# Performance work log

Hardware: AMD Instinct MI355X
Metric: run time of the kernel (lower is better)

The kernel has to match this reference:

```python
import jax, jax.numpy as jnp
import numpy as np

K = 30          # hard-coded in Hypergraph.from_feature_kNN(ft, k=30)
BN_EPS = 1e-5   # BatchNorm1d eval mode, running_mean=0, running_var=1


def setup_inputs() -> dict:
    key = jax.random.key(0)
    ks = jax.random.split(key, 3)
    B, C, H, W = 8, 64, 56, 56
    hid = 32
    return {
        "x": jax.random.normal(ks[0], (B, C, H, W), jnp.float32),
        "w1": jax.random.normal(ks[1], (C, hid), jnp.float32) / np.sqrt(C).astype(np.float32),
        "b1": jnp.zeros((hid,), jnp.float32),
        "g1": jnp.ones((hid,), jnp.float32),
        "be1": jnp.zeros((hid,), jnp.float32),
        "w2": jax.random.normal(ks[2], (hid, C), jnp.float32) / np.sqrt(hid).astype(np.float32),
        "b2": jnp.zeros((C,), jnp.float32),
        "g2": jnp.ones((C,), jnp.float32),
        "be2": jnp.zeros((C,), jnp.float32),
    }


def _knn_idx(ft, k):
    # squared euclidean distances via gram trick; same ordering as torch.cdist
    sq = jnp.sum(ft * ft, axis=1)
    d2 = sq[:, None] + sq[None, :] - 2.0 * (ft @ ft.T)   # [L, L]
    _, idx = jax.lax.top_k(-d2, k)                        # k smallest distances (incl. self)
    return idx                                            # [L, k] -> hyperedge e = kNN of vertex e


def _v2v_mean(X, nbr):
    # hg.v2v(X, aggr="mean"): v2e mean then e2v mean over the kNN incidence structure
    L, k = nbr.shape
    F = X.shape[1]
    Y = jnp.mean(X[nbr], axis=1)                                        # v2e: [L_edges, F]
    seg = nbr.reshape(-1)                                               # vertex nbr[e,j] belongs to edge e
    vals = jnp.broadcast_to(Y[:, None, :], (L, k, F)).reshape(L * k, F)
    s = jax.ops.segment_sum(vals, seg, num_segments=L)                  # e2v sum
    dv = jax.ops.segment_sum(jnp.ones((L * k,), X.dtype), seg, num_segments=L)
    return s / jnp.maximum(dv, 1.0)[:, None]                            # e2v mean


def _bn_eval(x, g, b):
    # BatchNorm1d in eval: running_mean=0, running_var=1
    return x * (g * np.float32(1.0 / np.sqrt(1.0 + BN_EPS))) + b


def reference(x, w1, b1, g1, be1, w2, b2, g2, be2):
    B, C, H, W = x.shape
    L = H * W
    xf = x.reshape(B, L, C)  # faithful raw x.view(B, L, C) (no transpose in source)

    def per_sample(ft):
        nbr = _knn_idx(ft, K)
        # HGNNPConv 1: theta -> bn -> v2v(mean) -> relu (dropout off in eval)
        h = _bn_eval(ft @ w1 + b1, g1, be1)
        h = jax.nn.relu(_v2v_mean(h, nbr))
        # HGNNPConv 2 (is_last): theta -> bn -> v2v(mean), no act/drop
        h = _bn_eval(h @ w2 + b2, g2, be2)
        return _v2v_mean(h, nbr)  # [L, C]

    outs = jax.vmap(per_sample)(xf)      # [B, L, C]
    return outs.reshape(B, -1, H, W)     # faithful raw outs.view(B, -1, H, W)
```

## Files before the change

kernel.cpp:

```cpp
#include <hip/hip_runtime.h>
#include <math.h>


namespace {

constexpr int cB = 8;
constexpr int cL = 3136;
constexpr int cC = 64;
constexpr int cH = 32;
constexpr int cK = 30;
constexpr int NV = cB * cL;
constexpr int QD = 10;
constexpr float BN_SC = 0.99999500003749964f;

typedef __bf16 bf16x8 __attribute__((ext_vector_type(8)));
typedef float floatx4 __attribute__((ext_vector_type(4)));

union BU {
  __bf16 b[2];
  unsigned u;
};

__device__ inline unsigned umin2(unsigned a, unsigned b) { return a < b ? a : b; }
__device__ inline unsigned umax2(unsigned a, unsigned b) { return a > b ? a : b; }
__device__ inline unsigned umin3(unsigned a, unsigned b, unsigned c) {
  return umin2(umin2(a, b), c);
}
__device__ inline float bf16lo(unsigned u) { return __uint_as_float(u << 16); }
__device__ inline float bf16hi(unsigned u) {
  return __uint_as_float(u & 0xFFFF0000u);
}

__device__ inline unsigned bclean64(unsigned v, int ln) {
#pragma unroll
  for (int off = 32; off; off >>= 1) {
    unsigned p = (unsigned)__shfl_xor((int)v, off);
    v = (ln & off) ? umax2(v, p) : umin2(v, p);
  }
  return v;
}

__global__ __launch_bounds__(256) void k_splitth(
    const float* __restrict__ x, const float* __restrict__ w1,
    const float* __restrict__ b1, const float* __restrict__ g1,
    const float* __restrict__ be1, ushort* __restrict__ xhi,
    ushort* __restrict__ xlo, float* __restrict__ sqf,
    int* __restrict__ cnt, int* __restrict__ cur, __bf16* __restrict__ h1) {
  __shared__ float w1s[cC * cH];
  __shared__ float xs[8 * 64];
  const int t = threadIdx.x;
  const int v0 = blockIdx.x * 8;
  for (int n = t; n < cC * cH; n += 256) w1s[n] = w1[n];
  {
    float2 xv = reinterpret_cast<const float2*>(x + (size_t)v0 * 64)[t];
    xs[2 * t] = xv.x;
    xs[2 * t + 1] = xv.y;
    BU hh, ll;
    hh.b[0] = (__bf16)xv.x;
    hh.b[1] = (__bf16)xv.y;
    ll.b[0] = (__bf16)(xv.x - (float)hh.b[0]);
    ll.b[1] = (__bf16)(xv.y - (float)hh.b[1]);
    reinterpret_cast<unsigned*>(xhi)[(size_t)v0 * 32 + t] = hh.u;
    reinterpret_cast<unsigned*>(xlo)[(size_t)v0 * 32 + t] = ll.u;
    float ss = xv.x * xv.x + xv.y * xv.y;
#pragma unroll
    for (int off = 1; off < 32; off <<= 1) ss += __shfl_xor(ss, off);
    if ((t & 31) == 0) sqf[v0 + (t >> 5)] = ss * 1024.f + 262144.f;
  }
  if (t < 8) {
    cnt[v0 + t] = 0;
    cur[v0 + t] = 0;
  }
  __syncthreads();
  const int r = t >> 5, f = t & 31;
  float s = 0.f;
#pragma unroll
  for (int k = 0; k < cC; ++k) s = fmaf(xs[r * 64 + k], w1s[k * cH + f], s);
  h1[(size_t)(v0 + r) * cH + f] =
      (__bf16)((s + b1[f]) * (g1[f] * BN_SC) + be1[f]);
}

__global__ __launch_bounds__(128, 4) void k_sweep(
    const ushort* __restrict__ xhi, const ushort* __restrict__ xlo,
    const float* __restrict__ sqf, unsigned* __restrict__ candq) {
  const int ib = blockIdx.x, qt = blockIdx.y, b = blockIdx.z;
  const int r0 = ib * 32;
  const int jb0 = qt * 1568;
  const int ntile = 49;
  const size_t bbase = (size_t)b * cL;

  __shared__ ushort aHi[32 * 72], aLo[32 * 72];
  __shared__ ushort bHi[32 * 72], bLo[32 * 72];
  __shared__ float sqJs[32];

  const int t  = threadIdx.x;
  const int ln = t & 63;
  const int w  = t >> 6;
  const int tx = ln & 15;
  const int qd = ln >> 4;

#pragma unroll
  for (int it = 0; it < 2; ++it) {
    int idx = t + 128 * it;
    int r = idx >> 3, blk = idx & 7;
    *reinterpret_cast<uint4*>(&aHi[r * 72 + blk * 8]) =
        *reinterpret_cast<const uint4*>(&xhi[(bbase + r0 + r) * 64 + blk * 8]);
    *reinterpret_cast<uint4*>(&aLo[r * 72 + blk * 8]) =
        *reinterpret_cast<const uint4*>(&xlo[(bbase + r0 + r) * 64 + blk * 8]);
  }
  __syncthreads();

  bf16x8 aH[2], aL[2];
#pragma unroll
  for (int kk = 0; kk < 2; ++kk) {
    aH[kk] = *reinterpret_cast<const bf16x8*>(
        &aHi[(w * 16 + tx) * 72 + kk * 32 + qd * 8]);
    aL[kk] = *reinterpret_cast<const bf16x8*>(
        &aLo[(w * 16 + tx) * 72 + kk * 32 + qd * 8]);
  }

  unsigned q[4][QD];
#pragma unroll
  for (int e = 0; e < 4; ++e)
#pragma unroll
    for (int k = 0; k < QD; ++k) q[e][k] = 0xFFFFFFFFu;

  const int pr  = (t + 0)   >> 3, pblk  = (t + 0)   & 7;
  const int pr1 = (t + 128) >> 3, pblk1 = (t + 128) & 7;
  uint4 pH0, pH1, pL0, pL1;
  float pS = 0.f;
  {
    const int jb = jb0;
    pH0 = *reinterpret_cast<const uint4*>(&xhi[(bbase + jb + pr) * 64 + pblk * 8]);
    pL0 = *reinterpret_cast<const uint4*>(&xlo[(bbase + jb + pr) * 64 + pblk * 8]);
    pH1 = *reinterpret_cast<const uint4*>(&xhi[(bbase + jb + pr1) * 64 + pblk1 * 8]);
    pL1 = *reinterpret_cast<const uint4*>(&xlo[(bbase + jb + pr1) * 64 + pblk1 * 8]);
    if (t < 32) pS = sqf[bbase + jb + t];
  }

  for (int st = 0; st < ntile; ++st) {
    __syncthreads();
    *reinterpret_cast<uint4*>(&bHi[pr * 72 + pblk * 8])   = pH0;
    *reinterpret_cast<uint4*>(&bLo[pr * 72 + pblk * 8])   = pL0;
    *reinterpret_cast<uint4*>(&bHi[pr1 * 72 + pblk1 * 8]) = pH1;
    *reinterpret_cast<uint4*>(&bLo[pr1 * 72 + pblk1 * 8]) = pL1;
    if (t < 32) sqJs[t] = pS;
    __syncthreads();

    if (st + 1 < ntile) {
      const int jb = jb0 + (st + 1) * 32;
      pH0 = *reinterpret_cast<const uint4*>(&xhi[(bbase + jb + pr) * 64 + pblk * 8]);
      pL0 = *reinterpret_cast<const uint4*>(&xlo[(bbase + jb + pr) * 64 + pblk * 8]);
      pH1 = *reinterpret_cast<const uint4*>(&xhi[(bbase + jb + pr1) * 64 + pblk1 * 8]);
      pL1 = *reinterpret_cast<const uint4*>(&xlo[(bbase + jb + pr1) * 64 + pblk1 * 8]);
      if (t < 32) pS = sqf[bbase + jb + t];
    }
    __builtin_amdgcn_sched_barrier(0);

    unsigned pk[2][4];
#pragma unroll
    for (int f = 0; f < 2; ++f) {
      const int bro = (f * 16 + tx) * 72 + qd * 8;
      bf16x8 bh0 = *reinterpret_cast<const bf16x8*>(&bHi[bro]);
      bf16x8 bh1 = *reinterpret_cast<const bf16x8*>(&bHi[bro + 32]);
      bf16x8 bl0 = *reinterpret_cast<const bf16x8*>(&bLo[bro]);
      bf16x8 bl1 = *reinterpret_cast<const bf16x8*>(&bLo[bro + 32]);
      floatx4 acc = {0.f, 0.f, 0.f, 0.f};
      acc = __builtin_amdgcn_mfma_f32_16x16x32_bf16(aH[0], bh0, acc, 0, 0, 0);
      acc = __builtin_amdgcn_mfma_f32_16x16x32_bf16(aH[1], bh1, acc, 0, 0, 0);
      acc = __builtin_amdgcn_mfma_f32_16x16x32_bf16(aH[0], bl0, acc, 0, 0, 0);
      acc = __builtin_amdgcn_mfma_f32_16x16x32_bf16(aH[1], bl1, acc, 0, 0, 0);
      acc = __builtin_amdgcn_mfma_f32_16x16x32_bf16(aL[0], bh0, acc, 0, 0, 0);
      acc = __builtin_amdgcn_mfma_f32_16x16x32_bf16(aL[1], bh1, acc, 0, 0, 0);
      const float sjs = sqJs[f * 16 + tx];
      const unsigned col = (unsigned)(jb0 + st * 32 + f * 16 + tx);
#pragma unroll
      for (int e = 0; e < 4; ++e) {
        float qf = fmaf(acc[e], -2048.f, sjs);
        qf = fminf(fmaxf(qf, 0.f), 1048575.f);
        pk[f][e] = ((unsigned)qf << 12) | col;
      }
    }

#pragma unroll
    for (int e = 0; e < 4; ++e) {
      unsigned a0 = umin2(pk[0][e], pk[1][e]);
      unsigned a1 = umax2(pk[0][e], pk[1][e]);
#pragma unroll
      for (int i = QD - 1; i >= 2; --i)
        q[e][i] = umin3(q[e][i], umax2(q[e][i - 1], a0),
                        umax2(q[e][i - 2], a1));
      q[e][1] = umin3(q[e][1], umax2(q[e][0], a0), a1);
      q[e][0] = umin3(q[e][0], a0, a1);
    }
  }

  unsigned* cr[4];
#pragma unroll
  for (int e = 0; e < 4; ++e)
    cr[e] = candq + (bbase + r0 + w * 16 + qd * 4 + e) * 80 + qt * 40;
  for (int it = 0; it < 40; ++it) {
    unsigned h0 = q[0][0], h1 = q[1][0], h2 = q[2][0], h3 = q[3][0];
    unsigned m0 = h0, m1 = h1, m2 = h2, m3 = h3;
#pragma unroll
    for (int off = 1; off < 16; off <<= 1) {
      m0 = umin2(m0, (unsigned)__shfl_xor((int)m0, off));
      m1 = umin2(m1, (unsigned)__shfl_xor((int)m1, off));
      m2 = umin2(m2, (unsigned)__shfl_xor((int)m2, off));
      m3 = umin2(m3, (unsigned)__shfl_xor((int)m3, off));
    }
    if (tx == 0) {
      cr[0][it] = m0;
      cr[1][it] = m1;
      cr[2][it] = m2;
      cr[3][it] = m3;
    }
    if (h0 == m0) {
#pragma unroll
      for (int k = 0; k < QD - 1; ++k) q[0][k] = q[0][k + 1];
      q[0][QD - 1] = 0xFFFFFFFFu;
    }
    if (h1 == m1) {
#pragma unroll
      for (int k = 0; k < QD - 1; ++k) q[1][k] = q[1][k + 1];
      q[1][QD - 1] = 0xFFFFFFFFu;
    }
    if (h2 == m2) {
#pragma unroll
      for (int k = 0; k < QD - 1; ++k) q[2][k] = q[2][k + 1];
      q[2][QD - 1] = 0xFFFFFFFFu;
    }
    if (h3 == m3) {
#pragma unroll
      for (int k = 0; k < QD - 1; ++k) q[3][k] = q[3][k + 1];
      q[3][QD - 1] = 0xFFFFFFFFu;
    }
  }
}

__global__ __launch_bounds__(256) void k_rescore(
    const float* __restrict__ x, const unsigned* __restrict__ candq,
    const __bf16* __restrict__ h1, int* __restrict__ nbr,
    int* __restrict__ cnt, __bf16* __restrict__ Y1) {
  const int w  = threadIdx.x >> 6;
  const int ln = threadIdx.x & 63;
  const size_t row = (size_t)blockIdx.x * 4 + w;
  const size_t bvert = row - (row % cL);

  const unsigned* cq = candq + row * 80;
  unsigned A = (ln < 40) ? cq[ln]      : 0xFFFFFFFFu;
  unsigned B = (ln < 40) ? cq[40 + ln] : 0xFFFFFFFFu;

  unsigned g = umin2(A, (unsigned)__shfl((int)B, 63 - ln));
  g = bclean64(g, ln);

  const unsigned qv = g >> 12;
  const int col = min((int)(g & 0xFFFu), cL - 1);

  unsigned q29 = (unsigned)__shfl((int)qv, 29);
  unsigned q30 = (unsigned)__shfl((int)qv, 30);
  int myc = col;
  if (!(q30 > q29 + 6)) {
    float4 xi[16];
    const float4* xi4 = reinterpret_cast<const float4*>(x + row * 64);
#pragma unroll
    for (int c = 0; c < 16; ++c) xi[c] = xi4[c];
    double dv = 1e300;
    if (ln < 40) {
      const float4* xj4 =
          reinterpret_cast<const float4*>(x + (bvert + col) * 64);
      double ax = 0.0, ay = 0.0, az = 0.0, aw = 0.0;
#pragma unroll
      for (int c = 0; c < 16; ++c) {
        float4 xj = xj4[c];
        double d0 = (double)xi[c].x - (double)xj.x; ax = fma(d0, d0, ax);
        double d1 = (double)xi[c].y - (double)xj.y; ay = fma(d1, d1, ay);
        double d2 = (double)xi[c].z - (double)xj.z; az = fma(d2, d2, az);
        double d3 = (double)xi[c].w - (double)xj.w; aw = fma(d3, d3, aw);
      }
      dv = (ax + ay) + (az + aw);
    }
    int r2 = 0;
    for (int j = 0; j < 40; ++j) {
      double od = __shfl(dv, j);
      r2 += (od < dv || (od == dv && j < ln)) ? 1 : 0;
    }
    myc = __builtin_amdgcn_ds_permute(r2 << 2, col);
  }
  if (ln < cK) {
    nbr[row * cK + ln] = myc;
    atomicAdd(&cnt[bvert + myc], 1);
  }

  const unsigned* Xb = reinterpret_cast<const unsigned*>(h1 + bvert * cH);
  const int qg = ln >> 4, f2 = ln & 15;
  float s0 = 0.f, s1 = 0.f;
#pragma unroll
  for (int m = 0; m < 8; ++m) {
    int j = m * 4 + qg;
    int idx = __shfl(myc, j < cK ? j : 0);
    unsigned u = Xb[(size_t)idx * 16 + f2];
    bool ok = j < cK;
    s0 += ok ? bf16lo(u) : 0.f;
    s1 += ok ? bf16hi(u) : 0.f;
  }
  s0 += __shfl_xor(s0, 16);
  s1 += __shfl_xor(s1, 16);
  s0 += __shfl_xor(s0, 32);
  s1 += __shfl_xor(s1, 32);
  if (ln < 16) {
    BU cv;
    cv.b[0] = (__bf16)(s0 * (1.f / 30.f));
    cv.b[1] = (__bf16)(s1 * (1.f / 30.f));
    reinterpret_cast<unsigned*>(Y1)[row * 16 + f2] = cv.u;
  }
}

__global__ __launch_bounds__(1024) void k_scan(const int* __restrict__ cnt,
                                               int* __restrict__ rp) {
  const int b = blockIdx.x;
  const int* c = cnt + b * cL;
  int* r = rp + b * (cL + 1);
  const int t = threadIdx.x;
  const int ln = t & 63, w = t >> 6;

  int v[4];
  int s = 0;
#pragma unroll
  for (int i = 0; i < 4; ++i) {
    int idx = 4 * t + i;
    v[i] = (idx < cL) ? c[idx] : 0;
    s += v[i];
  }
  int inc = s;
#pragma unroll
  for (int off = 1; off < 64; off <<= 1) {
    int u = __shfl_up(inc, off);
    if (ln >= off) inc += u;
  }
  __shared__ int wsum[16];
  if (ln == 63) wsum[w] = inc;
  __syncthreads();
  int carry = 0;
#pragma unroll
  for (int i = 0; i < 16; ++i) carry += (i < w) ? wsum[i] : 0;

  int excl = carry + inc - s;
#pragma unroll
  for (int i = 0; i < 4; ++i) {
    int idx = 4 * t + i;
    if (idx < cL) r[idx] = excl;
    excl += v[i];
  }
  if (t == 1023) r[cL] = excl;
}

__global__ void k_fill(const int* __restrict__ nbr, const int* __restrict__ rp,
                       int* __restrict__ cur, int* __restrict__ el) {
  int g = blockIdx.x * 256 + threadIdx.x;
  if (g >= NV * cK) return;
  int b = g / (cL * cK);
  int e = (g / cK) % cL;
  int v = nbr[g];
  v = min(max(v, 0), cL - 1);
  int p = rp[b * (cL + 1) + v] + atomicAdd(&cur[b * cL + v], 1);
  p = min(max(p, 0), cL * cK - 1);
  el[(size_t)b * cL * cK + p] = e;
}

__global__ __launch_bounds__(256) void k_e2v_t2(const __bf16* __restrict__ Y,
                                                const int* __restrict__ rp,
                                                const int* __restrict__ el,
                                                const float* __restrict__ w2,
                                                const float* __restrict__ b2,
                                                const float* __restrict__ g2,
                                                const float* __restrict__ be2,
                                                __bf16* __restrict__ h2) {
  __shared__ float w2s[cH * cC];
  {
    int t = threadIdx.x;
    for (int n = t; n < cH * cC; n += 256) w2s[n] = w2[n];
  }
  const int w  = threadIdx.x >> 6;
  const int ln = threadIdx.x & 63;
  const size_t vr = (size_t)blockIdx.x * 4 + w;
  const size_t b  = vr / cL;
  const int v = (int)(vr % cL);
  const int* rpb = rp + b * (cL + 1);
  const int s0 = rpb[v];
  const int deg = rpb[v + 1] - s0;
  const int* elb = el + b * (size_t)cL * cK + s0;
  const __bf16* Yb = Y + b * cL * cH;
  const int hi = ln >> 5, f = ln & 31;
  float s = 0.f;

  for (int base = 0; base < deg; base += 64) {
    const int take = min(64, deg - base);
    const int eidx = elb[base + (ln < take ? ln : 0)];
    for (int j0 = 0; j0 < take; j0 += 16) {
      float acc = 0.f;
#pragma unroll
      for (int k2 = 0; k2 < 8; ++k2) {
        int j = j0 + 2 * k2 + hi;
        int e0 = __shfl(eidx, j < take ? j : 0);
        float y = (float)Yb[(size_t)e0 * cH + f];
        acc += (j < take) ? y : 0.f;
      }
      s += acc;
    }
  }
  __syncthreads();

  s += __shfl_xor(s, 32);
  float r = fmaxf(s / (float)deg, 0.f);

  float s2 = 0.f;
#pragma unroll 8
  for (int k = 0; k < cH; ++k) {
    float rk = __shfl(r, k);
    s2 = fmaf(rk, w2s[k * cC + ln], s2);
  }
  h2[vr * cC + ln] = (__bf16)((s2 + b2[ln]) * (g2[ln] * BN_SC) + be2[ln]);
}

__global__ __launch_bounds__(256) void k_v2e64(const __bf16* __restrict__ X,
                                               const int* __restrict__ nbr,
                                               __bf16* __restrict__ Y) {
  const int w  = threadIdx.x >> 6;
  const int ln = threadIdx.x & 63;
  const size_t er = (size_t)blockIdx.x * 4 + w;
  const size_t b  = er / cL;
  const unsigned* Xb = reinterpret_cast<const unsigned*>(X + b * cL * cC);
  const int nb_l = nbr[er * cK + (ln < cK ? ln : cK - 1)];
  const int half = ln >> 5, f2 = ln & 31;
  int idx[15];
#pragma unroll
  for (int m = 0; m < 15; ++m) idx[m] = __shfl(nb_l, 2 * m + half);
  unsigned v[15];
#pragma unroll
  for (int m = 0; m < 15; ++m) v[m] = Xb[(size_t)idx[m] * 32 + f2];
  float s0 = 0.f, s1 = 0.f;
#pragma unroll
  for (int m = 0; m < 15; ++m) {
    s0 += bf16lo(v[m]);
    s1 += bf16hi(v[m]);
  }
  s0 += __shfl_xor(s0, 32);
  s1 += __shfl_xor(s1, 32);
  if (half == 0) {
    BU cv;
    cv.b[0] = (__bf16)(s0 * (1.f / 30.f));
    cv.b[1] = (__bf16)(s1 * (1.f / 30.f));
    reinterpret_cast<unsigned*>(Y)[er * 32 + f2] = cv.u;
  }
}

__global__ __launch_bounds__(256) void k_e2v64(const __bf16* __restrict__ Y,
                                               const int* __restrict__ rp,
                                               const int* __restrict__ el,
                                               float* __restrict__ out) {
  const int w  = threadIdx.x >> 6;
  const int ln = threadIdx.x & 63;
  const size_t vr = (size_t)blockIdx.x * 4 + w;
  const size_t b  = vr / cL;
  const int v = (int)(vr % cL);
  const int* rpb = rp + b * (cL + 1);
  const int s0r = rpb[v];
  const int deg = rpb[v + 1] - s0r;
  const int* elb = el + b * (size_t)cL * cK + s0r;
  const unsigned* Yb = reinterpret_cast<const unsigned*>(Y + b * cL * cC);
  const int half = ln >> 5, f2 = ln & 31;
  float s0 = 0.f, s1 = 0.f;

  for (int base = 0; base < deg; base += 64) {
    const int take = min(64, deg - base);
    const int eidx = elb[base + (ln < take ? ln : 0)];
    for (int j0 = 0; j0 < take; j0 += 16) {
      float a0 = 0.f, a1 = 0.f;
#pragma unroll
      for (int k2 = 0; k2 < 8; ++k2) {
        int j = j0 + 2 * k2 + half;
        int e0 = __shfl(eidx, j < take ? j : 0);
        unsigned u = Yb[(size_t)e0 * 32 + f2];
        bool ok = j < take;
        a0 += ok ? bf16lo(u) : 0.f;
        a1 += ok ? bf16hi(u) : 0.f;
      }
      s0 += a0;
      s1 += a1;
    }
  }
  s0 += __shfl_xor(s0, 32);
  s1 += __shfl_xor(s1, 32);
  float v0 = __shfl(s0, ln >> 1);
  float v1 = __shfl(s1, ln >> 1);
  out[vr * cC + ln] = ((ln & 1) ? v1 : v0) / (float)deg;
}

}

extern "C" void kernel_launch(void* const* d_in, const int* in_sizes, int n_in,
                              void* d_out, int out_size, void* d_ws,
                              size_t ws_size, hipStream_t stream) {
  (void)in_sizes; (void)n_in; (void)out_size; (void)ws_size;
  const float* x   = (const float*)d_in[0];
  const float* w1  = (const float*)d_in[1];
  const float* b1  = (const float*)d_in[2];
  const float* g1  = (const float*)d_in[3];
  const float* be1 = (const float*)d_in[4];
  const float* w2  = (const float*)d_in[5];
  const float* b2  = (const float*)d_in[6];
  const float* g2  = (const float*)d_in[7];
  const float* be2 = (const float*)d_in[8];
  float* out = (float*)d_out;

  char* base = (char*)d_ws;
  size_t off = 0;
  auto carve = [&](size_t bytes) {
    char* p = base + off;
    off += (bytes + 255) & ~(size_t)255;
    return p;
  };
  float* sqf = (float*)carve((size_t)NV * 4);
  int*   nbr = (int*)carve((size_t)NV * cK * 4);
  int*   rp  = (int*)carve((size_t)cB * (cL + 1) * 4);
  int*   cnt = (int*)carve((size_t)NV * 4);
  int*   cur = (int*)carve((size_t)NV * 4);
  char* RA = carve((size_t)NV * 64 * 2 * 2);
  ushort* xhi = (ushort*)RA;
  ushort* xlo = (ushort*)(RA + 3211264);
  int* el = (int*)RA;
  char* RC = carve(17661952);
  unsigned* candq = (unsigned*)RC;
  __bf16* h1 = (__bf16*)(RC + 8028160);
  __bf16* Y1 = (__bf16*)(RC + 9633792);
  __bf16* h2 = (__bf16*)(RC + 11239424);
  __bf16* Y2 = (__bf16*)(RC + 14450688);

  k_splitth<<<NV / 8, 256, 0, stream>>>(x, w1, b1, g1, be1, xhi, xlo, sqf,
                                        cnt, cur, h1);
  k_sweep<<<dim3(98, 2, cB), 128, 0, stream>>>(xhi, xlo, sqf, candq);
  k_rescore<<<NV / 4, 256, 0, stream>>>(x, candq, h1, nbr, cnt, Y1);

  k_scan<<<cB, 1024, 0, stream>>>(cnt, rp);
  k_fill<<<(NV * cK) / 256, 256, 0, stream>>>(nbr, rp, cur, el);

  k_e2v_t2<<<NV / 4, 256, 0, stream>>>(Y1, rp, el, w2, b2, g2, be2, h2);
  k_v2e64<<<NV / 4, 256, 0, stream>>>(h2, nbr, Y2);
  k_e2v64<<<NV / 4, 256, 0, stream>>>(Y2, rp, el, out);
}
```

Measured before the change: 373.5 us.

## Fuse post-kNN stages into one cooperative persistent kernel with grid syncs

Replaces the five launches for scan, CSR fill, e2v+theta2, v2e and final e2v with a single cooperative kernel of 1024 persistent blocks. The stages are separated by grid.sync() and each uses a grid-stride loop. This removes the launch gaps and kernel-boundary drains between the small stages. In exchange each stage is capped at 1024 resident blocks, the grid-wide barriers have their own cost, and the scan now runs on 256 threads instead of 1024.

```diff
diff --git a/kernel.cpp b/kernel.cpp
--- a/kernel.cpp
+++ b/kernel.cpp
@@ -1,5 +1,8 @@
 #include <hip/hip_runtime.h>
+#include <hip/hip_cooperative_groups.h>
 #include <math.h>
+
+namespace cg = cooperative_groups;
 
 
 namespace {
@@ -316,185 +319,170 @@
   }
 }
 
-__global__ __launch_bounds__(1024) void k_scan(const int* __restrict__ cnt,
-                                               int* __restrict__ rp) {
-  const int b = blockIdx.x;
-  const int* c = cnt + b * cL;
-  int* r = rp + b * (cL + 1);
-  const int t = threadIdx.x;
-  const int ln = t & 63, w = t >> 6;
-
-  int v[4];
-  int s = 0;
-#pragma unroll
-  for (int i = 0; i < 4; ++i) {
-    int idx = 4 * t + i;
-    v[i] = (idx < cL) ? c[idx] : 0;
-    s += v[i];
-  }
-  int inc = s;
-#pragma unroll
-  for (int off = 1; off < 64; off <<= 1) {
-    int u = __shfl_up(inc, off);
-    if (ln >= off) inc += u;
-  }
-  __shared__ int wsum[16];
-  if (ln == 63) wsum[w] = inc;
-  __syncthreads();
-  int carry = 0;
-#pragma unroll
-  for (int i = 0; i < 16; ++i) carry += (i < w) ? wsum[i] : 0;
-
-  int excl = carry + inc - s;
-#pragma unroll
-  for (int i = 0; i < 4; ++i) {
-    int idx = 4 * t + i;
-    if (idx < cL) r[idx] = excl;
-    excl += v[i];
-  }
-  if (t == 1023) r[cL] = excl;
-}
-
-__global__ void k_fill(const int* __restrict__ nbr, const int* __restrict__ rp,
-                       int* __restrict__ cur, int* __restrict__ el) {
-  int g = blockIdx.x * 256 + threadIdx.x;
-  if (g >= NV * cK) return;
-  int b = g / (cL * cK);
-  int e = (g / cK) % cL;
-  int v = nbr[g];
-  v = min(max(v, 0), cL - 1);
-  int p = rp[b * (cL + 1) + v] + atomicAdd(&cur[b * cL + v], 1);
-  p = min(max(p, 0), cL * cK - 1);
-  el[(size_t)b * cL * cK + p] = e;
-}
-
-__global__ __launch_bounds__(256) void k_e2v_t2(const __bf16* __restrict__ Y,
-                                                const int* __restrict__ rp,
-                                                const int* __restrict__ el,
-                                                const float* __restrict__ w2,
-                                                const float* __restrict__ b2,
-                                                const float* __restrict__ g2,
-                                                const float* __restrict__ be2,
-                                                __bf16* __restrict__ h2) {
+__global__ __launch_bounds__(256, 4) void k_post(
+    const int* __restrict__ cnt, int* __restrict__ rp,
+    const int* __restrict__ nbr, int* __restrict__ cur, int* __restrict__ el,
+    const __bf16* __restrict__ Y1, const float* __restrict__ w2,
+    const float* __restrict__ b2, const float* __restrict__ g2,
+    const float* __restrict__ be2, __bf16* __restrict__ h2,
+    __bf16* __restrict__ Y2, float* __restrict__ out) {
+  cg::grid_group grid = cg::this_grid();
   __shared__ float w2s[cH * cC];
-  {
-    int t = threadIdx.x;
-    for (int n = t; n < cH * cC; n += 256) w2s[n] = w2[n];
-  }
-  const int w  = threadIdx.x >> 6;
-  const int ln = threadIdx.x & 63;
-  const size_t vr = (size_t)blockIdx.x * 4 + w;
-  const size_t b  = vr / cL;
-  const int v = (int)(vr % cL);
-  const int* rpb = rp + b * (cL + 1);
-  const int s0 = rpb[v];
-  const int deg = rpb[v + 1] - s0;
-  const int* elb = el + b * (size_t)cL * cK + s0;
-  const __bf16* Yb = Y + b * cL * cH;
-  const int hi = ln >> 5, f = ln & 31;
-  float s = 0.f;
-
-  for (int base = 0; base < deg; base += 64) {
-    const int take = min(64, deg - base);
-    const int eidx = elb[base + (ln < take ? ln : 0)];
-    for (int j0 = 0; j0 < take; j0 += 16) {
-      float acc = 0.f;
-#pragma unroll
-      for (int k2 = 0; k2 < 8; ++k2) {
-        int j = j0 + 2 * k2 + hi;
-        int e0 = __shfl(eidx, j < take ? j : 0);
-        float y = (float)Yb[(size_t)e0 * cH + f];
-        acc += (j < take) ? y : 0.f;
+  __shared__ int wsum[4];
+  const int t  = threadIdx.x;
+  const int ln = t & 63;
+  const int w  = t >> 6;
+  for (int n = t; n < cH * cC; n += 256) w2s[n] = w2[n];
+
+  if (blockIdx.x < cB) {
+    const int b = blockIdx.x;
+    const int* c = cnt + b * cL;
+    int* r = rp + b * (cL + 1);
+    int v[13];
+    int s = 0;
+    const int base = t * 13;
+#pragma unroll
+    for (int i = 0; i < 13; ++i) {
+      int idx = base + i;
+      v[i] = (idx < cL) ? c[idx] : 0;
+      s += v[i];
+    }
+    int inc = s;
+#pragma unroll
+    for (int off = 1; off < 64; off <<= 1) {
+      int u = __shfl_up(inc, off);
+      if (ln >= off) inc += u;
+    }
+    if (ln == 63) wsum[w] = inc;
+    __syncthreads();
+    int carry = 0;
+#pragma unroll
+    for (int i = 0; i < 4; ++i) carry += (i < w) ? wsum[i] : 0;
+    int excl = carry + inc - s;
+#pragma unroll
+    for (int i = 0; i < 13; ++i) {
+      int idx = base + i;
+      if (idx < cL) r[idx] = excl;
+      excl += v[i];
+    }
+    if (t == 255) r[cL] = excl;
+  }
+  grid.sync();
+
+  for (int u = blockIdx.x; u < (NV * cK) / 256; u += (int)gridDim.x) {
+    int gidx = u * 256 + t;
+    int b = gidx / (cL * cK);
+    int e = (gidx / cK) % cL;
+    int v = nbr[gidx];
+    v = min(max(v, 0), cL - 1);
+    int p = rp[b * (cL + 1) + v] + atomicAdd(&cur[b * cL + v], 1);
+    p = min(max(p, 0), cL * cK - 1);
+    el[(size_t)b * cL * cK + p] = e;
+  }
+  grid.sync();
+
+  for (int u = blockIdx.x; u < NV / 4; u += (int)gridDim.x) {
+    const size_t vr = (size_t)u * 4 + w;
+    const size_t b  = vr / cL;
+    const int v = (int)(vr % cL);
+    const int* rpb = rp + b * (cL + 1);
+    const int s0 = rpb[v];
+    const int deg = rpb[v + 1] - s0;
+    const int* elb = el + b * (size_t)cL * cK + s0;
+    const __bf16* Yb = Y1 + b * cL * cH;
+    const int hi = ln >> 5, f = ln & 31;
+    float s = 0.f;
+    for (int base2 = 0; base2 < deg; base2 += 64) {
+      const int take = min(64, deg - base2);
+      const int eidx = elb[base2 + (ln < take ? ln : 0)];
+      for (int j0 = 0; j0 < take; j0 += 16) {
+        float acc = 0.f;
+#pragma unroll
+        for (int k2 = 0; k2 < 8; ++k2) {
+          int j = j0 + 2 * k2 + hi;
+          int e0 = __shfl(eidx, j < take ? j : 0);
+          float y = (float)Yb[(size_t)e0 * cH + f];
+          acc += (j < take) ? y : 0.f;
+        }
+        s += acc;
       }
-      s += acc;
-    }
-  }
-  __syncthreads();
-
-  s += __shfl_xor(s, 32);
-  float r = fmaxf(s / (float)deg, 0.f);
-
-  float s2 = 0.f;
+    }
+    s += __shfl_xor(s, 32);
+    float r = fmaxf(s / (float)deg, 0.f);
+    float s2 = 0.f;
 #pragma unroll 8
-  for (int k = 0; k < cH; ++k) {
-    float rk = __shfl(r, k);
-    s2 = fmaf(rk, w2s[k * cC + ln], s2);
-  }
-  h2[vr * cC + ln] = (__bf16)((s2 + b2[ln]) * (g2[ln] * BN_SC) + be2[ln]);
-}
-
-__global__ __launch_bounds__(256) void k_v2e64(const __bf16* __restrict__ X,
-                                               const int* __restrict__ nbr,
-                                               __bf16* __restrict__ Y) {
-  const int w  = threadIdx.x >> 6;
-  const int ln = threadIdx.x & 63;
-  const size_t er = (size_t)blockIdx.x * 4 + w;
-  const size_t b  = er / cL;
-  const unsigned* Xb = reinterpret_cast<const unsigned*>(X + b * cL * cC);
-  const int nb_l = nbr[er * cK + (ln < cK ? ln : cK - 1)];
-  const int half = ln >> 5, f2 = ln & 31;
-  int idx[15];
-#pragma unroll
-  for (int m = 0; m < 15; ++m) idx[m] = __shfl(nb_l, 2 * m + half);
-  unsigned v[15];
-#pragma unroll
-  for (int m = 0; m < 15; ++m) v[m] = Xb[(size_t)idx[m] * 32 + f2];
-  float s0 = 0.f, s1 = 0.f;
-#pragma unroll
-  for (int m = 0; m < 15; ++m) {
-    s0 += bf16lo(v[m]);
-    s1 += bf16hi(v[m]);
-  }
-  s0 += __shfl_xor(s0, 32);
-  s1 += __shfl_xor(s1, 32);
-  if (half == 0) {
-    BU cv;
-    cv.b[0] = (__bf16)(s0 * (1.f / 30.f));
-    cv.b[1] = (__bf16)(s1 * (1.f / 30.f));
-    reinterpret_cast<unsigned*>(Y)[er * 32 + f2] = cv.u;
-  }
-}
-
-__global__ __launch_bounds__(256) void k_e2v64(const __bf16* __restrict__ Y,
-                                               const int* __restrict__ rp,
-                                               const int* __restrict__ el,
-                                               float* __restrict__ out) {
-  const int w  = threadIdx.x >> 6;
-  const int ln = threadIdx.x & 63;
-  const size_t vr = (size_t)blockIdx.x * 4 + w;
-  const size_t b  = vr / cL;
-  const int v = (int)(vr % cL);
-  const int* rpb = rp + b * (cL + 1);
-  const int s0r = rpb[v];
-  const int deg = rpb[v + 1] - s0r;
-  const int* elb = el + b * (size_t)cL * cK + s0r;
-  const unsigned* Yb = reinterpret_cast<const unsigned*>(Y + b * cL * cC);
-  const int half = ln >> 5, f2 = ln & 31;
-  float s0 = 0.f, s1 = 0.f;
-
-  for (int base = 0; base < deg; base += 64) {
-    const int take = min(64, deg - base);
-    const int eidx = elb[base + (ln < take ? ln : 0)];
-    for (int j0 = 0; j0 < take; j0 += 16) {
-      float a0 = 0.f, a1 = 0.f;
-#pragma unroll
-      for (int k2 = 0; k2 < 8; ++k2) {
-        int j = j0 + 2 * k2 + half;
-        int e0 = __shfl(eidx, j < take ? j : 0);
-        unsigned u = Yb[(size_t)e0 * 32 + f2];
-        bool ok = j < take;
-        a0 += ok ? bf16lo(u) : 0.f;
-        a1 += ok ? bf16hi(u) : 0.f;
+    for (int k = 0; k < cH; ++k) {
+      float rk = __shfl(r, k);
+      s2 = fmaf(rk, w2s[k * cC + ln], s2);
+    }
+    h2[vr * cC + ln] = (__bf16)((s2 + b2[ln]) * (g2[ln] * BN_SC) + be2[ln]);
+  }
+  grid.sync();
+
+  for (int u = blockIdx.x; u < NV / 4; u += (int)gridDim.x) {
+    const size_t er = (size_t)u * 4 + w;
+    const size_t b  = er / cL;
+    const unsigned* Xb = reinterpret_cast<const unsigned*>(h2 + b * cL * cC);
+    const int nb_l = nbr[er * cK + (ln < cK ? ln : cK - 1)];
+    const int half = ln >> 5, f2 = ln & 31;
+    int idx[15];
+#pragma unroll
+    for (int m = 0; m < 15; ++m) idx[m] = __shfl(nb_l, 2 * m + half);
+    unsigned v[15];
+#pragma unroll
+    for (int m = 0; m < 15; ++m) v[m] = Xb[(size_t)idx[m] * 32 + f2];
+    float s0 = 0.f, s1 = 0.f;
+#pragma unroll
+    for (int m = 0; m < 15; ++m) {
+      s0 += bf16lo(v[m]);
+      s1 += bf16hi(v[m]);
+    }
+    s0 += __shfl_xor(s0, 32);
+    s1 += __shfl_xor(s1, 32);
+    if (half == 0) {
+      BU cv;
+      cv.b[0] = (__bf16)(s0 * (1.f / 30.f));
+      cv.b[1] = (__bf16)(s1 * (1.f / 30.f));
+      reinterpret_cast<unsigned*>(Y2)[er * 32 + f2] = cv.u;
+    }
+  }
+  grid.sync();
+
+  for (int u = blockIdx.x; u < NV / 4; u += (int)gridDim.x) {
+    const size_t vr = (size_t)u * 4 + w;
+    const size_t b  = vr / cL;
+    const int v = (int)(vr % cL);
+    const int* rpb = rp + b * (cL + 1);
+    const int s0r = rpb[v];
+    const int deg = rpb[v + 1] - s0r;
+    const int* elb = el + b * (size_t)cL * cK + s0r;
+    const unsigned* Yb = reinterpret_cast<const unsigned*>(Y2 + b * cL * cC);
+    const int half = ln >> 5, f2 = ln & 31;
+    float s0 = 0.f, s1 = 0.f;
+    for (int base2 = 0; base2 < deg; base2 += 64) {
+      const int take = min(64, deg - base2);
+      const int eidx = elb[base2 + (ln < take ? ln : 0)];
+      for (int j0 = 0; j0 < take; j0 += 16) {
+        float a0 = 0.f, a1 = 0.f;
+#pragma unroll
+        for (int k2 = 0; k2 < 8; ++k2) {
+          int j = j0 + 2 * k2 + half;
+          int e0 = __shfl(eidx, j < take ? j : 0);
+          unsigned uu = Yb[(size_t)e0 * 32 + f2];
+          bool ok = j < take;
+          a0 += ok ? bf16lo(uu) : 0.f;
+          a1 += ok ? bf16hi(uu) : 0.f;
+        }
+        s0 += a0;
+        s1 += a1;
       }
-      s0 += a0;
-      s1 += a1;
-    }
-  }
-  s0 += __shfl_xor(s0, 32);
-  s1 += __shfl_xor(s1, 32);
-  float v0 = __shfl(s0, ln >> 1);
-  float v1 = __shfl(s1, ln >> 1);
-  out[vr * cC + ln] = ((ln & 1) ? v1 : v0) / (float)deg;
+    }
+    s0 += __shfl_xor(s0, 32);
+    s1 += __shfl_xor(s1, 32);
+    float v0 = __shfl(s0, ln >> 1);
+    float v1 = __shfl(s1, ln >> 1);
+    out[vr * cC + ln] = ((ln & 1) ? v1 : v0) / (float)deg;
+  }
 }
 
 }
@@ -542,10 +530,10 @@
   k_sweep<<<dim3(98, 2, cB), 128, 0, stream>>>(xhi, xlo, sqf, candq);
   k_rescore<<<NV / 4, 256, 0, stream>>>(x, candq, h1, nbr, cnt, Y1);
 
-  k_scan<<<cB, 1024, 0, stream>>>(cnt, rp);
-  k_fill<<<(NV * cK) / 256, 256, 0, stream>>>(nbr, rp, cur, el);
-
-  k_e2v_t2<<<NV / 4, 256, 0, stream>>>(Y1, rp, el, w2, b2, g2, be2, h2);
-  k_v2e64<<<NV / 4, 256, 0, stream>>>(h2, nbr, Y2);
-  k_e2v64<<<NV / 4, 256, 0, stream>>>(Y2, rp, el, out);
-}
+  void* kargs[] = {(void*)&cnt, (void*)&rp,  (void*)&nbr, (void*)&cur,
+                   (void*)&el,  (void*)&Y1,  (void*)&w2,  (void*)&b2,
+                   (void*)&g2,  (void*)&be2, (void*)&h2,  (void*)&Y2,
+                   (void*)&out};
+  hipLaunchCooperativeKernel((const void*)k_post, dim3(1024), dim3(256),
+                             kargs, 0, stream);
+}
```

New measurement: 882.2 us. +136.2%, slower.
